# Kernel optimization log

Measured on AMD Instinct MI355X. Metric: run time of the kernel, lower is better.

Reference implementation:

```python
import jax, jax.numpy as jnp
import numpy as np

B, T, D = 2, 2048, 2048
Q_HEADS, KV_HEADS, HEAD_DIM = 16, 4, 128
ROPE_BASE = 10000.0


def _apply_rotary(x_nhd, positions_n):
    # x_nhd: (N, H, head_dim); half-split rotary embedding.
    half = x_nhd.shape[-1] // 2
    inv_freq = 1.0 / (ROPE_BASE ** (jnp.arange(half, dtype=jnp.float32) / half))
    ang = positions_n.astype(jnp.float32)[:, None] * inv_freq  # (N, half)
    cos = jnp.cos(ang)[:, None, :]  # (N, 1, half)
    sin = jnp.sin(ang)[:, None, :]
    x1, x2 = x_nhd[..., :half], x_nhd[..., half:]
    return jnp.concatenate([x1 * cos - x2 * sin, x1 * sin + x2 * cos], axis=-1)


def setup_inputs() -> dict:
    key = jax.random.key(0)
    ks = jax.random.split(key, 5)
    s_in = 1.0 / np.sqrt(D)
    s_o = 1.0 / np.sqrt(Q_HEADS * HEAD_DIM)
    x = jax.random.normal(ks[0], (B, T, D), dtype=jnp.float32)
    positions = jnp.broadcast_to(jnp.arange(T, dtype=jnp.int32), (B, T))
    wq = jax.random.normal(ks[1], (Q_HEADS * HEAD_DIM, D), dtype=jnp.float32) * s_in
    wk = jax.random.normal(ks[2], (KV_HEADS * HEAD_DIM, D), dtype=jnp.float32) * s_in
    wv = jax.random.normal(ks[3], (KV_HEADS * HEAD_DIM, D), dtype=jnp.float32) * s_in
    wo = jax.random.normal(ks[4], (D, Q_HEADS * HEAD_DIM), dtype=jnp.float32) * s_o
    return {"x": x, "positions": positions, "wq": wq, "wk": wk, "wv": wv, "wo": wo}


def reference(x, positions, wq, wk, wv, wo):
    bsz, tsz, _ = x.shape
    q = jnp.einsum('btd,od->bto', x, wq).reshape(bsz, tsz, Q_HEADS, HEAD_DIM)
    k = jnp.einsum('btd,od->bto', x, wk).reshape(bsz, tsz, KV_HEADS, HEAD_DIM)
    v = jnp.einsum('btd,od->bto', x, wv).reshape(bsz, tsz, KV_HEADS, HEAD_DIM)
    pos_flat = positions.reshape(-1)
    q = _apply_rotary(q.reshape(-1, Q_HEADS, HEAD_DIM), pos_flat).reshape(bsz, tsz, Q_HEADS, HEAD_DIM)
    k = _apply_rotary(k.reshape(-1, KV_HEADS, HEAD_DIM), pos_flat).reshape(bsz, tsz, KV_HEADS, HEAD_DIM)
    rep = Q_HEADS // KV_HEADS
    k = jnp.repeat(k, rep, axis=2)
    v = jnp.repeat(v, rep, axis=2)
    logits = jnp.einsum('bthd,bThd->bhtT', q, k) / jnp.sqrt(jnp.float32(HEAD_DIM))
    causal = jnp.tril(jnp.ones((tsz, tsz), dtype=bool))
    logits = jnp.where(causal[None, None], logits, -1e9)
    weights = jax.nn.softmax(logits, axis=-1)
    ctx = jnp.einsum('bhtT,bThd->bthd', weights, v).reshape(bsz, tsz, Q_HEADS * HEAD_DIM)
    return jnp.einsum('bto,do->btd', ctx, wo)
```

## Files before the change

kernel.cpp:

```cpp
#include <hip/hip_runtime.h>
#include <hip/hip_bf16.h>

typedef __bf16 bf16x8 __attribute__((ext_vector_type(8)));
typedef float  f32x4  __attribute__((ext_vector_type(4)));
typedef float  f32x16 __attribute__((ext_vector_type(16)));
typedef unsigned int u32x2 __attribute__((ext_vector_type(2)));

#define B_   2
#define T_   2048
#define D_   2048
#define QH_  16
#define KVH_ 4
#define HD_  128
#define BT_  (B_ * T_)
#define KVD_ 512
#define SCL  0.12751744f
#define NIF  -0.20762050593f

#define GLOAD_LDS16(g, l)                                        \
  __builtin_amdgcn_global_load_lds(                              \
      (const __attribute__((address_space(1))) void*)(g),        \
      (__attribute__((address_space(3))) void*)(l), 16, 0, 0)

#define SWZ(row)  ((((row) >> 3) ^ (row)) & 15)
#define SWZ8(row) ((((row) >> 3) ^ (row)) & 7)

__global__ __launch_bounds__(256) void cvt_all(
    const float* __restrict__ x, const float* __restrict__ wq,
    const float* __restrict__ wk, const float* __restrict__ wv,
    const float* __restrict__ wo, ushort* __restrict__ out) {
  const int i = blockIdx.x * 256 + threadIdx.x;
  int j = i;
  const float* src;
  float mul = 1.f;
  if (j < 2097152) { src = x; }
  else if ((j -= 2097152) < 1048576) { src = wq; mul = SCL; }
  else if ((j -= 1048576) < 262144)  { src = wk; }
  else if ((j -= 262144) < 262144)   { src = wv; }
  else { j -= 262144; src = wo; }
  float4 v = ((const float4*)src)[j];
  __hip_bfloat16 h0 = __float2bfloat16(v.x * mul);
  __hip_bfloat16 h1 = __float2bfloat16(v.y * mul);
  __hip_bfloat16 h2 = __float2bfloat16(v.z * mul);
  __hip_bfloat16 h3 = __float2bfloat16(v.w * mul);
  ushort4 o;
  o.x = *(ushort*)&h0; o.y = *(ushort*)&h1;
  o.z = *(ushort*)&h2; o.w = *(ushort*)&h3;
  ((ushort4*)out)[i] = o;
}

__global__ __launch_bounds__(256) void gemm_qkv(
    const ushort* __restrict__ X, const ushort* __restrict__ WQ,
    const ushort* __restrict__ WK, const ushort* __restrict__ WV,
    const int* __restrict__ positions,
    ushort* __restrict__ qo, ushort* __restrict__ ko, ushort* __restrict__ vo) {
  const int nb = blockIdx.x % 24;
  const int mb = blockIdx.x / 24;
  const int tid = threadIdx.x;
  const int wave = tid >> 6;
  const int lane = tid & 63;
  const int mrow = lane & 15;
  const int quad = lane >> 4;
  const int wm = wave >> 1;
  const int wn = wave & 1;
  const int m0 = mb * 128;
  const int K = D_;

  const ushort* Wg;
  if (nb < 16)      Wg = WQ + (size_t)nb * 128 * K;
  else if (nb < 20) Wg = WK + (size_t)(nb - 16) * 128 * K;
  else              Wg = WV + (size_t)(nb - 20) * 128 * K;

  __shared__ __align__(16) ushort smem[32768];
  ushort* Atp = smem;
  ushort* Btp = smem + 16384;

  f32x4 acc[4][4];
#pragma unroll
  for (int i = 0; i < 4; ++i)
#pragma unroll
    for (int j = 0; j < 4; ++j) acc[i][j] = (f32x4){0.f, 0.f, 0.f, 0.f};

  const ushort* Xg = X + (size_t)m0 * K;

  auto STAGE = [&](int buf, int k0) {
#pragma unroll
    for (int p = 0; p < 4; ++p) {
      const int c = p * 256 + tid;
      const int row = c >> 3;
      const int cc = (c & 7) ^ (row & 7);
      GLOAD_LDS16(Xg + (size_t)row * K + k0 + cc * 8,
                  Atp + (size_t)buf * 8192 + (size_t)(p * 256 + wave * 64) * 8);
      GLOAD_LDS16(Wg + (size_t)row * K + k0 + cc * 8,
                  Btp + (size_t)buf * 8192 + (size_t)(p * 256 + wave * 64) * 8);
    }
  };

  const int NT = K / 64;
  STAGE(0, 0);
  STAGE(1, 64);

  for (int t = 0; t < NT; ++t) {
    const int cur = t & 1;
    if (t + 2 < NT) asm volatile("s_waitcnt vmcnt(8)" ::: "memory");
    else            asm volatile("s_waitcnt vmcnt(0)" ::: "memory");
    __builtin_amdgcn_s_barrier();

    const ushort* Ac = Atp + (size_t)cur * 8192;
    const ushort* Bc = Btp + (size_t)cur * 8192;
#pragma unroll
    for (int s = 0; s < 2; ++s) {
      bf16x8 af[4], bfr[4];
#pragma unroll
      for (int mt = 0; mt < 4; ++mt) {
        const int row = wm * 64 + mt * 16 + mrow;
        af[mt] = *reinterpret_cast<const bf16x8*>(
            Ac + row * 64 + (((s * 4 + quad) ^ (row & 7)) * 8));
      }
#pragma unroll
      for (int nt = 0; nt < 4; ++nt) {
        const int row = wn * 64 + nt * 16 + mrow;
        bfr[nt] = *reinterpret_cast<const bf16x8*>(
            Bc + row * 64 + (((s * 4 + quad) ^ (row & 7)) * 8));
      }
#pragma unroll
      for (int mt = 0; mt < 4; ++mt)
#pragma unroll
        for (int nt = 0; nt < 4; ++nt)
          acc[mt][nt] = __builtin_amdgcn_mfma_f32_16x16x32_bf16(
              af[mt], bfr[nt], acc[mt][nt], 0, 0, 0);
    }

    asm volatile("s_waitcnt lgkmcnt(0)" ::: "memory");
    __builtin_amdgcn_s_barrier();
    if (t + 2 < NT) STAGE(cur, (t + 2) * 64);
  }

  if (nb < 20) {
    float* sC = (float*)smem;
#pragma unroll
    for (int mt = 0; mt < 4; ++mt)
#pragma unroll
      for (int nt = 0; nt < 4; ++nt) {
        const int colw = wn * 64 + nt * 16 + mrow;
        const int rl0 = wm * 64 + mt * 16 + quad * 4;
#pragma unroll
        for (int r = 0; r < 4; ++r)
          sC[(rl0 + r) * 128 + colw] = acc[mt][nt][r];
      }
    __syncthreads();

    ushort* outp; int ldo, colbase;
    if (nb < 16) { outp = qo; ldo = 2048; colbase = nb * 128; }
    else         { outp = ko; ldo = KVD_; colbase = (nb - 16) * 128; }

    const int col = tid & 63;
    const float inv = exp2f((float)col * NIF);
#pragma unroll 4
    for (int i = 0; i < 32; ++i) {
      const int row = i * 4 + (tid >> 6);
      const float x1 = sC[row * 128 + col];
      const float x2 = sC[row * 128 + col + 64];
      const float pos = (float)positions[m0 + row];
      const float ang = pos * inv;
      const float cc = cosf(ang);
      const float ss = sinf(ang);
      __hip_bfloat16 h1 = __float2bfloat16(x1 * cc - x2 * ss);
      __hip_bfloat16 h2 = __float2bfloat16(x1 * ss + x2 * cc);
      outp[(size_t)(m0 + row) * ldo + colbase + col] = *(ushort*)&h1;
      outp[(size_t)(m0 + row) * ldo + colbase + col + 64] = *(ushort*)&h2;
    }
  } else {
#pragma unroll
    for (int mt = 0; mt < 4; ++mt) {
#pragma unroll
      for (int nt = 0; nt < 4; ++nt) {
        const int colw = wn * 64 + nt * 16 + mrow;
        const int row0 = m0 + wm * 64 + mt * 16 + quad * 4;
        const int col = (nb - 20) * 128 + colw;
        const int bb = row0 >> 11;
        const int t0 = row0 & (T_ - 1);
        ushort4 s4;
#pragma unroll
        for (int r = 0; r < 4; ++r) {
          __hip_bfloat16 hh = __float2bfloat16(acc[mt][nt][r]);
          (&s4.x)[r] = *(ushort*)&hh;
        }
        *(ushort4*)(vo + ((size_t)(bb * KVD_ + col)) * T_ + t0) = s4;
      }
    }
  }
}

__global__ __launch_bounds__(256) void gemm_o(
    const ushort* __restrict__ X, const ushort* __restrict__ W,
    float* __restrict__ Y, int M, int N, int K) {
  const int nb128 = N >> 7;
  const int mb = blockIdx.x / nb128;
  const int nb = blockIdx.x % nb128;
  const int tid = threadIdx.x;
  const int wave = tid >> 6;
  const int lane = tid & 63;
  const int mrow = lane & 15;
  const int quad = lane >> 4;
  const int wm = wave >> 1;
  const int wn = wave & 1;
  const int m0 = mb * 128;
  const int n0 = nb * 128;

  __shared__ __align__(16) ushort At[2][128 * 64];
  __shared__ __align__(16) ushort Bt[2][128 * 64];

  f32x4 acc[4][4];
#pragma unroll
  for (int i = 0; i < 4; ++i)
#pragma unroll
    for (int j = 0; j < 4; ++j) acc[i][j] = (f32x4){0.f, 0.f, 0.f, 0.f};

  const ushort* Xg = X + (size_t)m0 * K;
  const ushort* Wg = W + (size_t)n0 * K;

  auto STAGE = [&](int buf, int k0) {
#pragma unroll
    for (int p = 0; p < 4; ++p) {
      const int c = p * 256 + tid;
      const int row = c >> 3;
      const int cc = (c & 7) ^ (row & 7);
      GLOAD_LDS16(Xg + (size_t)row * K + k0 + cc * 8,
                  At[buf] + (size_t)(p * 256 + wave * 64) * 8);
      GLOAD_LDS16(Wg + (size_t)row * K + k0 + cc * 8,
                  Bt[buf] + (size_t)(p * 256 + wave * 64) * 8);
    }
  };

  const int NT = K / 64;
  STAGE(0, 0);
  STAGE(1, 64);

  for (int t = 0; t < NT; ++t) {
    const int cur = t & 1;
    if (t + 2 < NT) asm volatile("s_waitcnt vmcnt(8)" ::: "memory");
    else            asm volatile("s_waitcnt vmcnt(0)" ::: "memory");
    __builtin_amdgcn_s_barrier();

    const ushort* Ac = At[cur];
    const ushort* Bc = Bt[cur];
#pragma unroll
    for (int s = 0; s < 2; ++s) {
      bf16x8 af[4], bfr[4];
#pragma unroll
      for (int mt = 0; mt < 4; ++mt) {
        const int row = wm * 64 + mt * 16 + mrow;
        af[mt] = *reinterpret_cast<const bf16x8*>(
            Ac + row * 64 + (((s * 4 + quad) ^ (row & 7)) * 8));
      }
#pragma unroll
      for (int nt = 0; nt < 4; ++nt) {
        const int row = wn * 64 + nt * 16 + mrow;
        bfr[nt] = *reinterpret_cast<const bf16x8*>(
            Bc + row * 64 + (((s * 4 + quad) ^ (row & 7)) * 8));
      }
#pragma unroll
      for (int mt = 0; mt < 4; ++mt)
#pragma unroll
        for (int nt = 0; nt < 4; ++nt)
          acc[mt][nt] = __builtin_amdgcn_mfma_f32_16x16x32_bf16(
              af[mt], bfr[nt], acc[mt][nt], 0, 0, 0);
    }

    asm volatile("s_waitcnt lgkmcnt(0)" ::: "memory");
    __builtin_amdgcn_s_barrier();
    if (t + 2 < NT) STAGE(cur, (t + 2) * 64);
  }

#pragma unroll
  for (int mt = 0; mt < 4; ++mt)
#pragma unroll
    for (int nt = 0; nt < 4; ++nt) {
      const int col = n0 + wn * 64 + nt * 16 + mrow;
      const int row0 = m0 + wm * 64 + mt * 16 + quad * 4;
#pragma unroll
      for (int r = 0; r < 4; ++r)
        Y[(size_t)(row0 + r) * N + col] = acc[mt][nt][r];
    }
}

static __device__ __forceinline__ unsigned pk2(float a, float b) {
  __hip_bfloat16 ha = __float2bfloat16(a);
  __hip_bfloat16 hb = __float2bfloat16(b);
  return (unsigned)(*(ushort*)&ha) | ((unsigned)(*(ushort*)&hb) << 16);
}

static __device__ __forceinline__ void hswap(unsigned& a, unsigned& b,
                                             const int hi) {
#if __has_builtin(__builtin_amdgcn_permlane32_swap)
  u32x2 r = __builtin_amdgcn_permlane32_swap(a, b, false, false);
  a = r.x;
  b = r.y;
#else
  unsigned s = __shfl_xor(hi ? a : b, 32, 64);
  unsigned na = hi ? s : a;
  b = hi ? b : s;
  a = na;
#endif
}

__global__ __launch_bounds__(256, 2) void attn_mfma(
    const ushort* __restrict__ q, const ushort* __restrict__ k,
    const ushort* __restrict__ vt, ushort* __restrict__ ctx) {
  const int tid = threadIdx.x;
  const int wave = tid >> 6;
  const int lane = tid & 63;
  const int m5 = lane & 31;
  const int hi = lane >> 5;
  const int parity = wave & 1;
  const int hh = wave >> 1;

  const int pj = blockIdx.x & 31;
  const int g  = blockIdx.x >> 5;
  const int b   = g >> 3;
  const int hkv = (g >> 1) & 3;
  const int hp  = g & 1;
  const int hq  = hkv * 4 + hp * 2 + hh;

  __shared__ __align__(16) ushort smem[32768];
  __shared__ float lbuf[2][32];

  const ushort* kbase = k + ((size_t)b * T_ * KVH_ + hkv) * HD_;
  const ushort* vbase = vt + (size_t)(b * KVD_ + hkv * HD_) * T_;

  for (int job = 0; job < 2; ++job) {
    const int qt = job ? pj : 63 - pj;
    const int q0 = qt * 32;
    const int ns = (qt >> 1) + 1;

    const ushort* qrow =
        q + ((size_t)(b * T_ + q0 + m5) * QH_ + hq) * HD_ + hi * 8;
    bf16x8 qf[8];
#pragma unroll
    for (int c = 0; c < 8; ++c)
      qf[c] = *reinterpret_cast<const bf16x8*>(qrow + c * 16);

    f32x16 o4[4];
#pragma unroll
    for (int dt = 0; dt < 4; ++dt)
#pragma unroll
      for (int r = 0; r < 16; ++r) o4[dt][r] = 0.f;
    float ls = 0.f;

    auto STAGE = [&](int buf, int s) {
      const int j0 = s * 64;
      ushort* kb_ = smem + buf * 16384;
      ushort* vb_ = smem + buf * 16384 + 8192;
#pragma unroll
      for (int p = 0; p < 4; ++p) {
        const int c = p * 256 + tid;
        const int krow = c >> 4;
        const int kco = (c & 15) ^ SWZ(krow);
        GLOAD_LDS16(kbase + (size_t)(j0 + krow) * KVD_ + kco * 8,
                    kb_ + (size_t)(p * 256 + wave * 64) * 8);
      }
#pragma unroll
      for (int p = 0; p < 4; ++p) {
        const int c = p * 256 + tid;
        const int vrow = c >> 3;
        const int vco = (c & 7) ^ SWZ8(vrow);
        GLOAD_LDS16(vbase + (size_t)vrow * T_ + j0 + vco * 8,
                    vb_ + (size_t)(p * 256 + wave * 64) * 8);
      }
    };

    STAGE(0, 0);

    for (int s = 0; s < ns; ++s) {
      const int cur = s & 1;
      if (s + 1 < ns) {
        STAGE(cur ^ 1, s + 1);
        asm volatile("s_waitcnt vmcnt(8)" ::: "memory");
      } else {
        asm volatile("s_waitcnt vmcnt(0)" ::: "memory");
      }
      __builtin_amdgcn_s_barrier();

      const ushort* kt  = smem + cur * 16384;
      const ushort* vtl = smem + cur * 16384 + 8192;
      const int c32 = 2 * s + parity;

      if (c32 <= qt) {
        __builtin_amdgcn_s_setprio(1);
        f32x16 sa;
#pragma unroll
        for (int r = 0; r < 16; ++r) sa[r] = 0.f;
        const int rowk = parity * 32 + m5;
#pragma unroll
        for (int c = 0; c < 8; ++c) {
          const int ch = (2 * c + hi) ^ SWZ(rowk);
          bf16x8 kf =
              *reinterpret_cast<const bf16x8*>(kt + rowk * 128 + ch * 8);
          sa = __builtin_amdgcn_mfma_f32_32x32x16_bf16(kf, qf[c], sa, 0, 0, 0);
        }

        float p[16];
        if (c32 == qt) {
#pragma unroll
          for (int r = 0; r < 16; ++r) {
            const int roff = (r & 3) + 8 * (r >> 2) + 4 * hi;
            p[r] = (roff > m5) ? 0.f : exp2f(sa[r]);
          }
        } else {
#pragma unroll
          for (int r = 0; r < 16; ++r) p[r] = exp2f(sa[r]);
        }
#pragma unroll
        for (int r = 0; r < 16; ++r) ls += p[r];

        unsigned u0 = pk2(p[0], p[1]);   unsigned u1 = pk2(p[2], p[3]);
        unsigned u2 = pk2(p[4], p[5]);   unsigned u3 = pk2(p[6], p[7]);
        unsigned u4 = pk2(p[8], p[9]);   unsigned u5 = pk2(p[10], p[11]);
        unsigned u6 = pk2(p[12], p[13]); unsigned u7 = pk2(p[14], p[15]);
        hswap(u0, u2, hi); hswap(u1, u3, hi);
        hswap(u4, u6, hi); hswap(u5, u7, hi);

#pragma unroll
        for (int half = 0; half < 2; ++half) {
          union { unsigned w[4]; bf16x8 v; } pa;
          pa.w[0] = half ? u4 : u0;
          pa.w[1] = half ? u5 : u1;
          pa.w[2] = half ? u6 : u2;
          pa.w[3] = half ? u7 : u3;
          const int gc2 = parity * 4 + half * 2;
#pragma unroll
          for (int dt = 0; dt < 4; ++dt) {
            const int rowv = dt * 32 + m5;
            const int chv = (gc2 + hi) ^ SWZ8(rowv);
            bf16x8 vf =
                *reinterpret_cast<const bf16x8*>(vtl + rowv * 64 + chv * 8);
            o4[dt] = __builtin_amdgcn_mfma_f32_32x32x16_bf16(pa.v, vf, o4[dt],
                                                             0, 0, 0);
          }
        }
        __builtin_amdgcn_s_setprio(0);
      }

      asm volatile("s_waitcnt lgkmcnt(0)" ::: "memory");
      __builtin_amdgcn_s_barrier();
    }

    const float lt = ls + __shfl_xor(ls, 32, 64);
    float* sO = (float*)smem;
    if (parity) {
#pragma unroll
      for (int reg = 0; reg < 16; ++reg) {
        const int qrw = (reg & 3) + 8 * (reg >> 2) + 4 * hi;
#pragma unroll
        for (int dt = 0; dt < 4; ++dt)
          sO[hh * 4096 + qrw * 128 + dt * 32 + m5] = o4[dt][reg];
      }
      if (hi == 0) lbuf[hh][m5] = lt;
    }
    __syncthreads();
    if (!parity) {
      const float ltot = lt + lbuf[hh][m5];
#pragma unroll
      for (int reg = 0; reg < 16; ++reg) {
        const int qrw = (reg & 3) + 8 * (reg >> 2) + 4 * hi;
        const float rl = 1.f / __shfl(ltot, qrw, 64);
        ushort* op =
            ctx + ((size_t)(b * T_ + q0 + qrw) * QH_ + hq) * HD_ + m5;
#pragma unroll
        for (int dt = 0; dt < 4; ++dt) {
          const float ov =
              o4[dt][reg] + sO[hh * 4096 + qrw * 128 + dt * 32 + m5];
          __hip_bfloat16 hb = __float2bfloat16(ov * rl);
          op[dt * 32] = *(ushort*)&hb;
        }
      }
    }
    __syncthreads();
  }
}

extern "C" void kernel_launch(void* const* d_in, const int* in_sizes, int n_in,
                              void* d_out, int out_size, void* d_ws, size_t ws_size,
                              hipStream_t stream) {
  const float* x  = (const float*)d_in[0];
  const int* pos  = (const int*)d_in[1];
  const float* wq = (const float*)d_in[2];
  const float* wk = (const float*)d_in[3];
  const float* wv = (const float*)d_in[4];
  const float* wo = (const float*)d_in[5];

  ushort* xb  = (ushort*)d_ws;
  ushort* wqb = xb  + (size_t)8388608;
  ushort* wkb = wqb + (size_t)4194304;
  ushort* wvb = wkb + (size_t)1048576;
  ushort* wob = wvb + (size_t)1048576;
  ushort* qb  = wob + (size_t)4194304;
  ushort* kb  = qb  + (size_t)8388608;
  ushort* vtb = kb  + (size_t)2097152;
  ushort* ctx = xb;

  cvt_all<<<18432, 256, 0, stream>>>(x, wq, wk, wv, wo, (ushort*)d_ws);

  gemm_qkv<<<(BT_ / 128) * 24, 256, 0, stream>>>(
      xb, wqb, wkb, wvb, pos, qb, kb, vtb);

  attn_mfma<<<512, 256, 0, stream>>>(qb, kb, vtb, ctx);

  gemm_o<<<(BT_ / 128) * (D_ / 128), 256, 0, stream>>>(
      ctx, wob, (float*)d_out, BT_, D_, QH_ * HD_);
}
```

Before: 282.8 us.

## Halve QKV GEMM K-tile and LDS footprint to fit two blocks per CU

```diff
diff --git a/kernel.cpp b/kernel.cpp
--- a/kernel.cpp
+++ b/kernel.cpp
@@ -24,6 +24,7 @@
 
 #define SWZ(row)  ((((row) >> 3) ^ (row)) & 15)
 #define SWZ8(row) ((((row) >> 3) ^ (row)) & 7)
+#define SWZ4(row) (((row) >> 1) & 3)
 
 __global__ __launch_bounds__(256) void cvt_all(
     const float* __restrict__ x, const float* __restrict__ wq,
@@ -49,7 +50,7 @@
   ((ushort4*)out)[i] = o;
 }
 
-__global__ __launch_bounds__(256) void gemm_qkv(
+__global__ __launch_bounds__(256, 2) void gemm_qkv(
     const ushort* __restrict__ X, const ushort* __restrict__ WQ,
     const ushort* __restrict__ WK, const ushort* __restrict__ WV,
     const int* __restrict__ positions,
@@ -71,9 +72,9 @@
   else if (nb < 20) Wg = WK + (size_t)(nb - 16) * 128 * K;
   else              Wg = WV + (size_t)(nb - 20) * 128 * K;
 
-  __shared__ __align__(16) ushort smem[32768];
+  __shared__ __align__(16) ushort smem[16640];
   ushort* Atp = smem;
-  ushort* Btp = smem + 16384;
+  ushort* Btp = smem + 8192;
 
   f32x4 acc[4][4];
 #pragma unroll
@@ -85,90 +86,95 @@
 
   auto STAGE = [&](int buf, int k0) {
 #pragma unroll
-    for (int p = 0; p < 4; ++p) {
+    for (int p = 0; p < 2; ++p) {
       const int c = p * 256 + tid;
-      const int row = c >> 3;
-      const int cc = (c & 7) ^ (row & 7);
+      const int row = c >> 2;
+      const int cc = (c & 3) ^ SWZ4(row);
       GLOAD_LDS16(Xg + (size_t)row * K + k0 + cc * 8,
-                  Atp + (size_t)buf * 8192 + (size_t)(p * 256 + wave * 64) * 8);
+                  Atp + (size_t)buf * 4096 + (size_t)(p * 256 + wave * 64) * 8);
       GLOAD_LDS16(Wg + (size_t)row * K + k0 + cc * 8,
-                  Btp + (size_t)buf * 8192 + (size_t)(p * 256 + wave * 64) * 8);
+                  Btp + (size_t)buf * 4096 + (size_t)(p * 256 + wave * 64) * 8);
     }
   };
 
-  const int NT = K / 64;
+  const int NT = K / 32;
   STAGE(0, 0);
-  STAGE(1, 64);
+  STAGE(1, 32);
 
   for (int t = 0; t < NT; ++t) {
     const int cur = t & 1;
-    if (t + 2 < NT) asm volatile("s_waitcnt vmcnt(8)" ::: "memory");
+    if (t + 2 < NT) asm volatile("s_waitcnt vmcnt(4)" ::: "memory");
     else            asm volatile("s_waitcnt vmcnt(0)" ::: "memory");
     __builtin_amdgcn_s_barrier();
 
-    const ushort* Ac = Atp + (size_t)cur * 8192;
-    const ushort* Bc = Btp + (size_t)cur * 8192;
-#pragma unroll
-    for (int s = 0; s < 2; ++s) {
-      bf16x8 af[4], bfr[4];
-#pragma unroll
-      for (int mt = 0; mt < 4; ++mt) {
-        const int row = wm * 64 + mt * 16 + mrow;
-        af[mt] = *reinterpret_cast<const bf16x8*>(
-            Ac + row * 64 + (((s * 4 + quad) ^ (row & 7)) * 8));
-      }
-#pragma unroll
-      for (int nt = 0; nt < 4; ++nt) {
-        const int row = wn * 64 + nt * 16 + mrow;
-        bfr[nt] = *reinterpret_cast<const bf16x8*>(
-            Bc + row * 64 + (((s * 4 + quad) ^ (row & 7)) * 8));
-      }
-#pragma unroll
-      for (int mt = 0; mt < 4; ++mt)
-#pragma unroll
-        for (int nt = 0; nt < 4; ++nt)
-          acc[mt][nt] = __builtin_amdgcn_mfma_f32_16x16x32_bf16(
-              af[mt], bfr[nt], acc[mt][nt], 0, 0, 0);
-    }
+    const ushort* Ac = Atp + (size_t)cur * 4096;
+    const ushort* Bc = Btp + (size_t)cur * 4096;
+    bf16x8 af[4], bfr[4];
+#pragma unroll
+    for (int mt = 0; mt < 4; ++mt) {
+      const int row = wm * 64 + mt * 16 + mrow;
+      af[mt] = *reinterpret_cast<const bf16x8*>(
+          Ac + row * 32 + ((quad ^ SWZ4(row)) * 8));
+    }
+#pragma unroll
+    for (int nt = 0; nt < 4; ++nt) {
+      const int row = wn * 64 + nt * 16 + mrow;
+      bfr[nt] = *reinterpret_cast<const bf16x8*>(
+          Bc + row * 32 + ((quad ^ SWZ4(row)) * 8));
+    }
+#pragma unroll
+    for (int mt = 0; mt < 4; ++mt)
+#pragma unroll
+      for (int nt = 0; nt < 4; ++nt)
+        acc[mt][nt] = __builtin_amdgcn_mfma_f32_16x16x32_bf16(
+            af[mt], bfr[nt], acc[mt][nt], 0, 0, 0);
 
     asm volatile("s_waitcnt lgkmcnt(0)" ::: "memory");
     __builtin_amdgcn_s_barrier();
-    if (t + 2 < NT) STAGE(cur, (t + 2) * 64);
+    if (t + 2 < NT) STAGE(cur, (t + 2) * 32);
   }
 
   if (nb < 20) {
     float* sC = (float*)smem;
-#pragma unroll
-    for (int mt = 0; mt < 4; ++mt)
-#pragma unroll
-      for (int nt = 0; nt < 4; ++nt) {
-        const int colw = wn * 64 + nt * 16 + mrow;
-        const int rl0 = wm * 64 + mt * 16 + quad * 4;
-#pragma unroll
-        for (int r = 0; r < 4; ++r)
-          sC[(rl0 + r) * 128 + colw] = acc[mt][nt][r];
-      }
-    __syncthreads();
-
     ushort* outp; int ldo, colbase;
     if (nb < 16) { outp = qo; ldo = 2048; colbase = nb * 128; }
     else         { outp = ko; ldo = KVD_; colbase = (nb - 16) * 128; }
 
     const int col = tid & 63;
+    const int wv = tid >> 6;
     const float inv = exp2f((float)col * NIF);
+
+#pragma unroll
+    for (int rh = 0; rh < 2; ++rh) {
+      if (wm == rh) {
+#pragma unroll
+        for (int mt = 0; mt < 4; ++mt)
+#pragma unroll
+          for (int nt = 0; nt < 4; ++nt) {
+            const int colw = wn * 64 + nt * 16 + mrow;
+            const int r0 = mt * 16 + quad * 4;
+#pragma unroll
+            for (int r = 0; r < 4; ++r)
+              sC[(r0 + r) * 130 + colw] = acc[mt][nt][r];
+          }
+      }
+      __syncthreads();
 #pragma unroll 4
-    for (int i = 0; i < 32; ++i) {
-      const int row = i * 4 + (tid >> 6);
-      const float x1 = sC[row * 128 + col];
-      const float x2 = sC[row * 128 + col + 64];
-      const float pos = (float)positions[m0 + row];
-      const float ang = pos * inv;
-      const float cc = cosf(ang);
-      const float ss = sinf(ang);
-      __hip_bfloat16 h1 = __float2bfloat16(x1 * cc - x2 * ss);
-      __hip_bfloat16 h2 = __float2bfloat16(x1 * ss + x2 * cc);
-      outp[(size_t)(m0 + row) * ldo + colbase + col] = *(ushort*)&h1;
-      outp[(size_t)(m0 + row) * ldo + colbase + col + 64] = *(ushort*)&h2;
+      for (int i = 0; i < 16; ++i) {
+        const int rl = i * 4 + wv;
+        const int grow = m0 + rh * 64 + rl;
+        const float x1 = sC[rl * 130 + col];
+        const float x2 = sC[rl * 130 + col + 64];
+        const float pos = (float)positions[grow];
+        const float ang = pos * inv;
+        const float cc = cosf(ang);
+        const float ss = sinf(ang);
+        __hip_bfloat16 h1 = __float2bfloat16(x1 * cc - x2 * ss);
+        __hip_bfloat16 h2 = __float2bfloat16(x1 * ss + x2 * cc);
+        outp[(size_t)grow * ldo + colbase + col] = *(ushort*)&h1;
+        outp[(size_t)grow * ldo + colbase + col + 64] = *(ushort*)&h2;
+      }
+      __syncthreads();
     }
   } else {
 #pragma unroll
```

New measurement: 290.0 us. 2.5% more time.
